# Performance work log

Measured on AMD Instinct MI355X. Metric: run time of the kernel, lower is better.

Reference implementation:

```python
import jax, jax.numpy as jnp
from jax import lax
import numpy as np

T, B, H, I, O = 2048, 256, 512, 1, 1


def setup_inputs() -> dict:
    key = jax.random.key(0)
    k = jax.random.split(key, 7)
    scale = 1.0 / np.sqrt(H)  # pytorch uniform init bound
    u = lambda kk, sh: jax.random.uniform(kk, sh, jnp.float32, -scale, scale)
    return {
        "input_seq": jax.random.normal(k[0], (T, B), jnp.float32),
        "W_ih": u(k[1], (4 * H, I)),   # gate order: i, f, g, o
        "W_hh": u(k[2], (4 * H, H)),
        "b_ih": u(k[3], (4 * H,)),
        "b_hh": u(k[4], (4 * H,)),
        "W_lin": u(k[5], (O, H)),
        "b_lin": u(k[6], (O,)),
    }


def reference(input_seq, W_ih, W_hh, b_ih, b_hh, W_lin, b_lin):
    # input_seq: [T, B] -> unsqueeze to [T, B, 1]
    x = input_seq[:, :, None]
    # precompute input projection for all timesteps: [T, B, 4H]
    x_proj = jnp.einsum('tbi,gi->tbg', x, W_ih) + (b_ih + b_hh)

    h0 = jnp.zeros((B, H), input_seq.dtype)
    c0 = jnp.zeros((B, H), input_seq.dtype)

    def step(carry, xp):
        h, c = carry
        gates = xp + h @ W_hh.T  # [B, 4H]
        i, f, g, o = jnp.split(gates, 4, axis=-1)
        i = jax.nn.sigmoid(i)
        f = jax.nn.sigmoid(f)
        g = jnp.tanh(g)
        o = jax.nn.sigmoid(o)
        c = f * c + i * g
        h = o * jnp.tanh(c)
        return (h, c), None

    (h_last, _), _ = lax.scan(step, (h0, c0), x_proj)
    # linear head on last timestep's hidden state: [B, O]
    return h_last @ W_lin.T + b_lin
```

## Files before the change

### kernel.cpp

```cpp
#include <hip/hip_runtime.h>

#define T_STEPS 2048
#define BATCH   256
#define HID     512
#define NG      16
#define NB      16
#define RING    6
#define SENT    0x3C3C3C3C

typedef _Float16 half8 __attribute__((ext_vector_type(8)));
typedef float f32x4 __attribute__((ext_vector_type(4)));
typedef int int4v __attribute__((ext_vector_type(4)));

__device__ __forceinline__ float sigmoid_f(float v) {
    return 1.f / (1.f + __expf(-v));
}
__device__ __forceinline__ float tanh_f(float v) {
    float a = fabsf(v);
    float e = __expf(2.f * a);
    float r = 1.f - 2.f / (e + 1.f);
    return copysignf(r, v);
}

__global__ __launch_bounds__(256, 1) void lstm_persistent(
    const float* __restrict__ x,
    const float* __restrict__ Wih,
    const float* __restrict__ Whh,
    const float* __restrict__ bih,
    const float* __restrict__ bhh,
    const float* __restrict__ Wlin,
    _Float16* __restrict__ hbuf,
    float* __restrict__ partial)
{
    const int tid  = threadIdx.x;
    const int g    = blockIdx.x & 15;
    const int j    = blockIdx.x >> 4;
    const int wave = tid >> 6;
    const int lane = tid & 63;
    const int quad = lane >> 4;
    const int ln16 = lane & 15;

    __shared__ float lds_part[2][4][4][16][34];

    half8 bf[4][2][4];
    #pragma unroll
    for (int gt = 0; gt < 4; ++gt) {
        #pragma unroll
        for (int ch = 0; ch < 2; ++ch) {
            const float* wr = Whh + (size_t)(gt * 512 + j * 32 + ch * 16 + ln16) * HID;
            #pragma unroll
            for (int ksl = 0; ksl < 4; ++ksl) {
                int k0 = (wave * 4 + ksl) * 32 + quad * 8;
                half8 v;
                #pragma unroll
                for (int e = 0; e < 8; ++e) v[e] = (_Float16)wr[k0 + e];
                bf[gt][ch][ksl] = v;
            }
        }
    }

    const int row_e = tid >> 4;
    const int cp    = (tid & 15) * 2;

    float wxA[4], wxB[4], bsA[4], bsB[4];
    #pragma unroll
    for (int gt = 0; gt < 4; ++gt) {
        int r0 = gt * 512 + j * 32 + cp;
        wxA[gt] = Wih[r0];
        wxB[gt] = Wih[r0 + 1];
        bsA[gt] = bih[r0] + bhh[r0];
        bsB[gt] = bih[r0 + 1] + bhh[r0 + 1];
    }

    float c0 = 0.f, c1 = 0.f;
    float hl0 = 0.f, hl1 = 0.f;
    bool  dead = false;

    float x_cur = x[(size_t)g * 16 + row_e];

    int s_in = 0, s_out = 1, s_rst = 5;

    for (int t = 0; t < T_STEPS; ++t) {
        unsigned long long haddr = (unsigned long long)(
            (const char*)hbuf
            + ((size_t)s_in * (BATCH * HID) + (size_t)(g * 16 + ln16) * HID) * 2
            + wave * 256 + quad * 16);
        int4v h0, h1, h2, h3;
        {
            unsigned it = 0;
            for (;;) {
                asm volatile(
                    "global_load_dwordx4 %0, %4, off sc0 sc1\n\t"
                    "global_load_dwordx4 %1, %4, off offset:64 sc0 sc1\n\t"
                    "global_load_dwordx4 %2, %4, off offset:128 sc0 sc1\n\t"
                    "global_load_dwordx4 %3, %4, off offset:192 sc0 sc1\n\t"
                    "s_waitcnt vmcnt(0)"
                    : "=&v"(h0), "=&v"(h1), "=&v"(h2), "=&v"(h3)
                    : "v"(haddr) : "memory");
                bool ok = true;
                #pragma unroll
                for (int e = 0; e < 4; ++e) {
                    ok = ok && (h0[e] != (int)SENT) && (h1[e] != (int)SENT)
                            && (h2[e] != (int)SENT) && (h3[e] != (int)SENT);
                }
                if (__ballot(ok) == ~0ull || dead) break;
                if (++it > 100000000u) { dead = true; break; }
            }
        }

        float x_next = x[(size_t)(t + 1 < T_STEPS ? t + 1 : t) * BATCH + g * 16 + row_e];

        f32x4 acc[4][2];
        #pragma unroll
        for (int gt = 0; gt < 4; ++gt) {
            acc[gt][0] = (f32x4){0.f, 0.f, 0.f, 0.f};
            acc[gt][1] = (f32x4){0.f, 0.f, 0.f, 0.f};
        }
        #define KSTEP(ksl, hx) {                                                      \
            half8 af = __builtin_bit_cast(half8, hx);                                 \
            _Pragma("unroll")                                                         \
            for (int gt = 0; gt < 4; ++gt) {                                          \
                acc[gt][0] = __builtin_amdgcn_mfma_f32_16x16x32_f16(af, bf[gt][0][ksl], acc[gt][0], 0, 0, 0); \
                acc[gt][1] = __builtin_amdgcn_mfma_f32_16x16x32_f16(af, bf[gt][1][ksl], acc[gt][1], 0, 0, 0); \
            } }
        KSTEP(0, h0) KSTEP(1, h1) KSTEP(2, h2) KSTEP(3, h3)
        #undef KSTEP

        const int tb = t & 1;
        #pragma unroll
        for (int gt = 0; gt < 4; ++gt) {
            #pragma unroll
            for (int r = 0; r < 4; ++r) {
                lds_part[tb][wave][gt][quad * 4 + r][ln16]      = acc[gt][0][r];
                lds_part[tb][wave][gt][quad * 4 + r][16 + ln16] = acc[gt][1][r];
            }
        }
        __syncthreads();

        {
            unsigned long long radr = (unsigned long long)(
                (char*)hbuf
                + ((size_t)s_rst * (BATCH * HID)
                   + (size_t)(g * 16 + row_e) * HID + j * 32 + cp) * 2);
            unsigned sv = SENT;
            asm volatile("global_store_dword %0, %1, off sc0 sc1"
                         : : "v"(radr), "v"(sv) : "memory");
        }

        const float xin = x_cur;
        float sA[4] = {0.f, 0.f, 0.f, 0.f};
        float sB[4] = {0.f, 0.f, 0.f, 0.f};
        #pragma unroll
        for (int w = 0; w < 4; ++w) {
            #pragma unroll
            for (int gt = 0; gt < 4; ++gt) {
                float2 v = *(const float2*)&lds_part[tb][w][gt][row_e][cp];
                sA[gt] += v.x;
                sB[gt] += v.y;
            }
        }
        float hv0, hv1;
        {
            float gi = sA[0] + xin * wxA[0] + bsA[0];
            float gf = sA[1] + xin * wxA[1] + bsA[1];
            float gg = sA[2] + xin * wxA[2] + bsA[2];
            float go = sA[3] + xin * wxA[3] + bsA[3];
            float iv = sigmoid_f(gi), fv = sigmoid_f(gf), gv = tanh_f(gg), ov = sigmoid_f(go);
            c0 = fv * c0 + iv * gv;
            hv0 = ov * tanh_f(c0);
        }
        {
            float gi = sB[0] + xin * wxB[0] + bsB[0];
            float gf = sB[1] + xin * wxB[1] + bsB[1];
            float gg = sB[2] + xin * wxB[2] + bsB[2];
            float go = sB[3] + xin * wxB[3] + bsB[3];
            float iv = sigmoid_f(gi), fv = sigmoid_f(gf), gv = tanh_f(gg), ov = sigmoid_f(go);
            c1 = fv * c1 + iv * gv;
            hv1 = ov * tanh_f(c1);
        }
        hl0 = hv0; hl1 = hv1;

        {
            _Float16 p0 = (_Float16)hv0, p1 = (_Float16)hv1;
            unsigned hbits = ((unsigned)__builtin_bit_cast(unsigned short, p1) << 16)
                           |  (unsigned)__builtin_bit_cast(unsigned short, p0);
            unsigned long long sadr = (unsigned long long)(
                (char*)hbuf
                + ((size_t)s_out * (BATCH * HID)
                   + (size_t)(g * 16 + row_e) * HID + j * 32 + cp) * 2);
            asm volatile("global_store_dword %0, %1, off sc0 sc1"
                         : : "v"(sadr), "v"(hbits) : "memory");
        }
        asm volatile("s_waitcnt vmcnt(0)" ::: "memory");

        x_cur = x_next;
        s_rst = s_in;
        s_in  = s_out;
        s_out = (s_out + 1 == RING) ? 0 : s_out + 1;
    }

    float p = hl0 * Wlin[j * 32 + cp] + hl1 * Wlin[j * 32 + cp + 1];
    #pragma unroll
    for (int off = 8; off; off >>= 1) p += __shfl_down(p, off, 16);
    if ((tid & 15) == 0) partial[(size_t)j * BATCH + g * 16 + row_e] = p;
}

__global__ void lstm_finalize(const float* __restrict__ partial,
                              const float* __restrict__ blin,
                              float* __restrict__ out)
{
    int b = threadIdx.x;
    float s = blin[0];
    #pragma unroll
    for (int jj = 0; jj < NG; ++jj) s += partial[(size_t)jj * BATCH + b];
    out[b] = s;
}

extern "C" void kernel_launch(void* const* d_in, const int* in_sizes, int n_in,
                              void* d_out, int out_size, void* d_ws, size_t ws_size,
                              hipStream_t stream) {
    const float* x    = (const float*)d_in[0];
    const float* Wih  = (const float*)d_in[1];
    const float* Whh  = (const float*)d_in[2];
    const float* bih  = (const float*)d_in[3];
    const float* bhh  = (const float*)d_in[4];
    const float* Wlin = (const float*)d_in[5];
    const float* blin = (const float*)d_in[6];

    char* ws = (char*)d_ws;
    _Float16* hbuf    = (_Float16*)ws;
    float*    partial = (float*)(ws + (2 << 20));

    const size_t slot_bytes = (size_t)BATCH * HID * sizeof(_Float16);
    hipMemsetAsync(hbuf, 0, slot_bytes, stream);
    hipMemsetAsync((char*)hbuf + slot_bytes, 0x3C, (RING - 1) * slot_bytes, stream);

    lstm_persistent<<<dim3(256), dim3(256), 0, stream>>>(
        x, Wih, Whh, bih, bhh, Wlin, hbuf, partial);
    lstm_finalize<<<dim3(1), dim3(256), 0, stream>>>(partial, blin, (float*)d_out);
}
```

Baseline: 4.382 ms.

## Double-buffer sentinel polling, vectorize h stores, drop per-step store drain

Replaces the blocking poll of the hidden-state ring with two in-flight load batches, so the next poll overlaps the check of the previous one, and latches each 16-byte chunk as soon as it is valid. The sentinel reset and h publication now use one dwordx4 store per four lanes, with h values gathered by shuffles. The trailing vmcnt(0) after the stores is removed and __syncthreads becomes a raw lgkmcnt wait plus s_barrier. The LDS row pad also changes from 34 to 36. Risks: weaker ordering guarantees between sentinel reset and h stores without the drain, more memory traffic from redundant polls, and a much smaller deadlock timeout.

```diff
diff --git a/kernel.cpp b/kernel.cpp
--- a/kernel.cpp
+++ b/kernel.cpp
@@ -21,6 +21,28 @@
     float r = 1.f - 2.f / (e + 1.f);
     return copysignf(r, v);
 }
+__device__ __forceinline__ bool gvalid(int4v p) {
+    return p[0] != (int)SENT && p[1] != (int)SENT &&
+           p[2] != (int)SENT && p[3] != (int)SENT;
+}
+
+#define ISSUE4(a,b,c,d)                                                       \
+    asm volatile(                                                             \
+        "global_load_dwordx4 %0, %4, off sc0 sc1\n\t"                         \
+        "global_load_dwordx4 %1, %4, off offset:64 sc0 sc1\n\t"               \
+        "global_load_dwordx4 %2, %4, off offset:128 sc0 sc1\n\t"              \
+        "global_load_dwordx4 %3, %4, off offset:192 sc0 sc1"                  \
+        : "=&v"(a), "=&v"(b), "=&v"(c), "=&v"(d)                              \
+        : "v"(haddr) : "memory")
+
+#define WAITBIND4(a,b,c,d)                                                    \
+    asm volatile("s_waitcnt vmcnt(4)"                                         \
+        : "+v"(a), "+v"(b), "+v"(c), "+v"(d) :: "memory")
+
+#define DRAINALL()                                                            \
+    asm volatile("s_waitcnt vmcnt(0)"                                         \
+        : "+v"(pA0), "+v"(pA1), "+v"(pA2), "+v"(pA3),                         \
+          "+v"(pB0), "+v"(pB1), "+v"(pB2), "+v"(pB3) :: "memory")
 
 __global__ __launch_bounds__(256, 1) void lstm_persistent(
     const float* __restrict__ x,
@@ -40,7 +62,7 @@
     const int quad = lane >> 4;
     const int ln16 = lane & 15;
 
-    __shared__ float lds_part[2][4][4][16][34];
+    __shared__ float lds_part[2][4][4][16][36];
 
     half8 bf[4][2][4];
     #pragma unroll
@@ -78,6 +100,7 @@
 
     float x_cur = x[(size_t)g * 16 + row_e];
 
+    const int4v sent4 = {(int)SENT, (int)SENT, (int)SENT, (int)SENT};
     int s_in = 0, s_out = 1, s_rst = 5;
 
     for (int t = 0; t < T_STEPS; ++t) {
@@ -85,28 +108,32 @@
             (const char*)hbuf
             + ((size_t)s_in * (BATCH * HID) + (size_t)(g * 16 + ln16) * HID) * 2
             + wave * 256 + quad * 16);
+        int4v pA0, pA1, pA2, pA3, pB0, pB1, pB2, pB3;
         int4v h0, h1, h2, h3;
+        bool v0 = false, v1 = false, v2 = false, v3 = false;
+        ISSUE4(pA0, pA1, pA2, pA3);
+        ISSUE4(pB0, pB1, pB2, pB3);
         {
             unsigned it = 0;
             for (;;) {
-                asm volatile(
-                    "global_load_dwordx4 %0, %4, off sc0 sc1\n\t"
-                    "global_load_dwordx4 %1, %4, off offset:64 sc0 sc1\n\t"
-                    "global_load_dwordx4 %2, %4, off offset:128 sc0 sc1\n\t"
-                    "global_load_dwordx4 %3, %4, off offset:192 sc0 sc1\n\t"
-                    "s_waitcnt vmcnt(0)"
-                    : "=&v"(h0), "=&v"(h1), "=&v"(h2), "=&v"(h3)
-                    : "v"(haddr) : "memory");
-                bool ok = true;
-                #pragma unroll
-                for (int e = 0; e < 4; ++e) {
-                    ok = ok && (h0[e] != (int)SENT) && (h1[e] != (int)SENT)
-                            && (h2[e] != (int)SENT) && (h3[e] != (int)SENT);
-                }
-                if (__ballot(ok) == ~0ull || dead) break;
-                if (++it > 100000000u) { dead = true; break; }
-            }
-        }
+                WAITBIND4(pA0, pA1, pA2, pA3);
+                if (!v0 && gvalid(pA0)) { h0 = pA0; v0 = true; }
+                if (!v1 && gvalid(pA1)) { h1 = pA1; v1 = true; }
+                if (!v2 && gvalid(pA2)) { h2 = pA2; v2 = true; }
+                if (!v3 && gvalid(pA3)) { h3 = pA3; v3 = true; }
+                if (__ballot(v0 && v1 && v2 && v3) == ~0ull || dead) break;
+                if (++it > 1000000u) { dead = true; break; }
+                ISSUE4(pA0, pA1, pA2, pA3);
+                WAITBIND4(pB0, pB1, pB2, pB3);
+                if (!v0 && gvalid(pB0)) { h0 = pB0; v0 = true; }
+                if (!v1 && gvalid(pB1)) { h1 = pB1; v1 = true; }
+                if (!v2 && gvalid(pB2)) { h2 = pB2; v2 = true; }
+                if (!v3 && gvalid(pB3)) { h3 = pB3; v3 = true; }
+                if (__ballot(v0 && v1 && v2 && v3) == ~0ull) break;
+                ISSUE4(pB0, pB1, pB2, pB3);
+            }
+        }
+        DRAINALL();
 
         float x_next = x[(size_t)(t + 1 < T_STEPS ? t + 1 : t) * BATCH + g * 16 + row_e];
 
@@ -135,16 +162,15 @@
                 lds_part[tb][wave][gt][quad * 4 + r][16 + ln16] = acc[gt][1][r];
             }
         }
-        __syncthreads();
-
-        {
+        asm volatile("s_waitcnt lgkmcnt(0)\n\ts_barrier" ::: "memory");
+
+        if ((lane & 3) == 0) {
             unsigned long long radr = (unsigned long long)(
                 (char*)hbuf
                 + ((size_t)s_rst * (BATCH * HID)
                    + (size_t)(g * 16 + row_e) * HID + j * 32 + cp) * 2);
-            unsigned sv = SENT;
-            asm volatile("global_store_dword %0, %1, off sc0 sc1"
-                         : : "v"(radr), "v"(sv) : "memory");
+            asm volatile("global_store_dwordx4 %0, %1, off sc0 sc1"
+                         : : "v"(radr), "v"(sent4) : "memory");
         }
 
         const float xin = x_cur;
@@ -184,14 +210,19 @@
             _Float16 p0 = (_Float16)hv0, p1 = (_Float16)hv1;
             unsigned hbits = ((unsigned)__builtin_bit_cast(unsigned short, p1) << 16)
                            |  (unsigned)__builtin_bit_cast(unsigned short, p0);
-            unsigned long long sadr = (unsigned long long)(
-                (char*)hbuf
-                + ((size_t)s_out * (BATCH * HID)
-                   + (size_t)(g * 16 + row_e) * HID + j * 32 + cp) * 2);
-            asm volatile("global_store_dword %0, %1, off sc0 sc1"
-                         : : "v"(sadr), "v"(hbits) : "memory");
-        }
-        asm volatile("s_waitcnt vmcnt(0)" ::: "memory");
+            int4v pk;
+            #pragma unroll
+            for (int e = 0; e < 4; ++e)
+                pk[e] = __shfl((int)hbits, (lane & ~3) + e, 64);
+            if ((lane & 3) == 0) {
+                unsigned long long sadr = (unsigned long long)(
+                    (char*)hbuf
+                    + ((size_t)s_out * (BATCH * HID)
+                       + (size_t)(g * 16 + row_e) * HID + j * 32 + cp) * 2);
+                asm volatile("global_store_dwordx4 %0, %1, off sc0 sc1"
+                             : : "v"(sadr), "v"(pk) : "memory");
+            }
+        }
 
         x_cur = x_next;
         s_rst = s_in;
```

New measurement: 6.288 ms. 43.5% more time.

## Prefetch next-step hidden state speculatively and trim sentinel reset stores

Applied to the files above, without the earlier changes.

The next timestep's h slice is now loaded early, before the gate math and h store of the current step, and checked when the next iteration begins. Only if any sentinel remains does it fall back to the spin loop, which hides some of the cross-block handoff latency. Sentinel resets are issued as one dwordx4 store per four lanes, the end-of-step vmcnt wait is dropped, __syncthreads becomes a raw lgkmcnt wait plus barrier, and the LDS row is padded to 36. The early probe often reads data that is not ready yet and then costs an extra reload, and the deadlock iteration cap is lowered.

```diff
diff --git a/kernel.cpp b/kernel.cpp
--- a/kernel.cpp
+++ b/kernel.cpp
@@ -21,6 +21,23 @@
     float r = 1.f - 2.f / (e + 1.f);
     return copysignf(r, v);
 }
+__device__ __forceinline__ bool gvalid(int4v p) {
+    return p[0] != (int)SENT && p[1] != (int)SENT &&
+           p[2] != (int)SENT && p[3] != (int)SENT;
+}
+
+#define PROBE(addr)                                                           \
+    asm volatile(                                                             \
+        "global_load_dwordx4 %0, %4, off sc0 sc1\n\t"                         \
+        "global_load_dwordx4 %1, %4, off offset:64 sc0 sc1\n\t"               \
+        "global_load_dwordx4 %2, %4, off offset:128 sc0 sc1\n\t"              \
+        "global_load_dwordx4 %3, %4, off offset:192 sc0 sc1"                  \
+        : "=&v"(q0), "=&v"(q1), "=&v"(q2), "=&v"(q3)                          \
+        : "v"(addr) : "memory")
+
+#define WAITQ()                                                               \
+    asm volatile("s_waitcnt vmcnt(0)"                                         \
+        : "+v"(q0), "+v"(q1), "+v"(q2), "+v"(q3) :: "memory")
 
 __global__ __launch_bounds__(256, 1) void lstm_persistent(
     const float* __restrict__ x,
@@ -40,7 +57,7 @@
     const int quad = lane >> 4;
     const int ln16 = lane & 15;
 
-    __shared__ float lds_part[2][4][4][16][34];
+    __shared__ float lds_part[2][4][4][16][36];
 
     half8 bf[4][2][4];
     #pragma unroll
@@ -78,15 +95,24 @@
 
     float x_cur = x[(size_t)g * 16 + row_e];
 
+    const int4v sent4 = {(int)SENT, (int)SENT, (int)SENT, (int)SENT};
     int s_in = 0, s_out = 1, s_rst = 5;
 
+    const unsigned long long lane_base = (unsigned long long)(
+        (const char*)hbuf + ((size_t)(g * 16 + ln16) * HID) * 2
+        + wave * 256 + quad * 16);
+    const unsigned long long slot_stride = (unsigned long long)BATCH * HID * 2;
+
+    int4v q0, q1, q2, q3;
+    PROBE(lane_base);
+
     for (int t = 0; t < T_STEPS; ++t) {
-        unsigned long long haddr = (unsigned long long)(
-            (const char*)hbuf
-            + ((size_t)s_in * (BATCH * HID) + (size_t)(g * 16 + ln16) * HID) * 2
-            + wave * 256 + quad * 16);
-        int4v h0, h1, h2, h3;
-        {
+        const unsigned long long haddr = lane_base + (unsigned long long)s_in * slot_stride;
+
+        WAITQ();
+        int4v h0 = q0, h1 = q1, h2 = q2, h3 = q3;
+        bool allv = gvalid(h0) && gvalid(h1) && gvalid(h2) && gvalid(h3);
+        if (__ballot(allv) != ~0ull) {
             unsigned it = 0;
             for (;;) {
                 asm volatile(
@@ -97,14 +123,9 @@
                     "s_waitcnt vmcnt(0)"
                     : "=&v"(h0), "=&v"(h1), "=&v"(h2), "=&v"(h3)
                     : "v"(haddr) : "memory");
-                bool ok = true;
-                #pragma unroll
-                for (int e = 0; e < 4; ++e) {
-                    ok = ok && (h0[e] != (int)SENT) && (h1[e] != (int)SENT)
-                            && (h2[e] != (int)SENT) && (h3[e] != (int)SENT);
-                }
+                bool ok = gvalid(h0) && gvalid(h1) && gvalid(h2) && gvalid(h3);
                 if (__ballot(ok) == ~0ull || dead) break;
-                if (++it > 100000000u) { dead = true; break; }
+                if (++it > 2000000u) { dead = true; break; }
             }
         }
 
@@ -135,16 +156,20 @@
                 lds_part[tb][wave][gt][quad * 4 + r][16 + ln16] = acc[gt][1][r];
             }
         }
-        __syncthreads();
-
-        {
+        asm volatile("s_waitcnt lgkmcnt(0)\n\ts_barrier" ::: "memory");
+
+        if ((lane & 3) == 0) {
             unsigned long long radr = (unsigned long long)(
                 (char*)hbuf
                 + ((size_t)s_rst * (BATCH * HID)
                    + (size_t)(g * 16 + row_e) * HID + j * 32 + cp) * 2);
-            unsigned sv = SENT;
-            asm volatile("global_store_dword %0, %1, off sc0 sc1"
-                         : : "v"(radr), "v"(sv) : "memory");
+            asm volatile("global_store_dwordx4 %0, %1, off sc0 sc1"
+                         : : "v"(radr), "v"(sent4) : "memory");
+        }
+
+        {
+            const unsigned long long naddr = lane_base + (unsigned long long)s_out * slot_stride;
+            PROBE(naddr);
         }
 
         const float xin = x_cur;
@@ -191,13 +216,13 @@
             asm volatile("global_store_dword %0, %1, off sc0 sc1"
                          : : "v"(sadr), "v"(hbits) : "memory");
         }
-        asm volatile("s_waitcnt vmcnt(0)" ::: "memory");
 
         x_cur = x_next;
         s_rst = s_in;
         s_in  = s_out;
         s_out = (s_out + 1 == RING) ? 0 : s_out + 1;
     }
+    WAITQ();
 
     float p = hl0 * Wlin[j * 32 + cp] + hl1 * Wlin[j * 32 + cp + 1];
     #pragma unroll
```

After: 7.166 ms. +63.5%, slower.
